# Kernel tuning notes

Hardware: AMD Instinct MI355X
Metric: run time of the kernel (lower is better)

The kernel has to match this reference:

```python
import jax, jax.numpy as jnp
import numpy as np

MARGIN = 1.0
EPS = 1e-12  # safe sqrt/normalize clamp; used entries have magnitude >> EPS


def _normalize(x):
    return x / jnp.maximum(jnp.linalg.norm(x, axis=-1, keepdims=True), EPS)


def _cdist(x, y):
    # Pairwise L2 distances, matches torch.cdist(p=2)
    sq = (jnp.sum(x * x, axis=-1)[:, None]
          + jnp.sum(y * y, axis=-1)[None, :]
          - 2.0 * (x @ y.T))
    return jnp.sqrt(jnp.maximum(sq, EPS))


def setup_inputs() -> dict:
    key = jax.random.key(0)
    k1, k2, k3 = jax.random.split(key, 3)
    B, P, D = 4096, 2, 256
    anchor = jax.random.normal(k1, (B, D), dtype=jnp.float32)
    positive = jax.random.normal(k2, (B, P, D), dtype=jnp.float32)
    labels = jax.random.randint(k3, (B,), 0, 200)
    return {"anchor": anchor, "positive": positive, "labels": labels}


def reference(anchor, positive, labels):
    a = _normalize(anchor)            # [B, D]
    p = _normalize(positive)          # [B, P, D]
    B = a.shape[0]
    all_labels = jnp.concatenate([labels, labels])           # [2B]
    neg_mask = all_labels[None, :] != labels[:, None]        # [B, 2B]
    idx = jnp.arange(B)
    losses = []
    for v in range(p.shape[1]):  # loop over small fixed num_positives
        feats = jnp.concatenate([a, p[:, v]], axis=0)        # [2B, D]
        dist = _cdist(feats, feats)                          # [2B, 2B]
        pos_dist = dist[idx, idx + B]                        # [B]
        # hard negative mining: min distance over different-label columns
        neg_dist = jnp.min(jnp.where(neg_mask, dist[:B], jnp.inf), axis=1)  # [B]
        losses.append(jnp.maximum(pos_dist - neg_dist + MARGIN, 0.0))
    return jnp.mean(jnp.stack(losses))
```

## Files before the change

kernel.cpp:

```cpp
#include <hip/hip_runtime.h>
#include <hip/hip_bf16.h>

#define NB    4096
#define ND    256
#define NP    2
#define TOT   (NB * 3)
#define RB    256
#define NCHUNK 48
#define COLS_PER_CHUNK (TOT / NCHUNK)
#define TILES (COLS_PER_CHUNK / 16)
#define PITCH 264
#define NEG_INIT (-4.0f)

typedef float f32x4 __attribute__((ext_vector_type(4)));

#define WS_F_OFF    0
#define WS_POS_OFF  (TOT * RB)
#define WS_PART_OFF (WS_POS_OFF + NB * NP * 4)

__global__ void norm_pos_kernel(const float* __restrict__ anchor,
                                const float* __restrict__ positive,
                                unsigned char* __restrict__ F,
                                float* __restrict__ posArr) {
    int wid = threadIdx.x >> 6, lane = threadIdx.x & 63;
    int row = blockIdx.x * 4 + wid;
    if (row < NB) {
        const float* src = anchor + (size_t)row * ND;
        float4 x = *(const float4*)(src + lane * 4);
        float ss = x.x * x.x + x.y * x.y + x.z * x.z + x.w * x.w;
        #pragma unroll
        for (int m = 1; m < 64; m <<= 1) ss += __shfl_xor(ss, m, 64);
        float inv = 1.0f / fmaxf(sqrtf(ss), 1e-12f);
        int pk = __builtin_amdgcn_cvt_pk_fp8_f32(x.x * inv, x.y * inv, 0, false);
        pk = __builtin_amdgcn_cvt_pk_fp8_f32(x.z * inv, x.w * inv, pk, true);
        *(int*)(F + (size_t)row * RB + lane * 4) = pk;
    } else {
        int q = row - NB;
        int v = q >> 12;
        int j = q & (NB - 1);
        const float* sp = positive + (size_t)(j * NP + v) * ND;
        const float* sa = anchor + (size_t)j * ND;
        float4 xp = *(const float4*)(sp + lane * 4);
        float4 xa = *(const float4*)(sa + lane * 4);
        float sspv = xp.x * xp.x + xp.y * xp.y + xp.z * xp.z + xp.w * xp.w;
        float ssa  = xa.x * xa.x + xa.y * xa.y + xa.z * xa.z + xa.w * xa.w;
        float dot  = xa.x * xp.x + xa.y * xp.y + xa.z * xp.z + xa.w * xp.w;
        #pragma unroll
        for (int m = 1; m < 64; m <<= 1) {
            sspv += __shfl_xor(sspv, m, 64);
            ssa  += __shfl_xor(ssa, m, 64);
            dot  += __shfl_xor(dot, m, 64);
        }
        float invp = 1.0f / fmaxf(sqrtf(sspv), 1e-12f);
        int pk = __builtin_amdgcn_cvt_pk_fp8_f32(xp.x * invp, xp.y * invp, 0, false);
        pk = __builtin_amdgcn_cvt_pk_fp8_f32(xp.z * invp, xp.w * invp, pk, true);
        *(int*)(F + (size_t)row * RB + lane * 4) = pk;
        if (lane == 0) {
            float inva = 1.0f / fmaxf(sqrtf(ssa), 1e-12f);
            float dn = dot * inva * invp;
            float sq = 2.0f - 2.0f * dn;
            posArr[j * NP + v] = sqrtf(fmaxf(sq, 1e-12f));
        }
    }
}

__global__ __launch_bounds__(256) void gram_max_kernel(
        const unsigned char* __restrict__ F,
        const int* __restrict__ labels,
        float* __restrict__ partials) {
    __shared__ unsigned char lds[2][16 * PITCH];
    __shared__ int slab[COLS_PER_CHUNK];
    int tid = threadIdx.x;
    int wid = tid >> 6, lane = tid & 63;
    int l15 = lane & 15, quad = lane >> 4;

    int id = blockIdx.x;
    int chunk = id >> 4;
    int rbi   = id & 15;

    int rowBase = rbi * 256 + wid * 64;
    int col0 = chunk * COLS_PER_CHUNK;
    int part = col0 >> 12;
    const unsigned char* Fb = F;

    slab[tid] = labels[(col0 & (NB - 1)) + tid];

    int scol = tid >> 4, sseg = tid & 15;

    long af[4][8];
    #pragma unroll
    for (int s = 0; s < 4; ++s) {
        const unsigned char* ar = Fb + (size_t)(rowBase + s * 16 + l15) * RB + quad * 8;
        #pragma unroll
        for (int kk = 0; kk < 8; ++kk)
            af[s][kk] = *(const long*)(ar + kk * 32);
    }
    unsigned rlp[4];
    #pragma unroll
    for (int s = 0; s < 4; ++s) {
        const int* lb = labels + rowBase + s * 16 + quad * 4;
        rlp[s] = (unsigned)lb[0] | ((unsigned)lb[1] << 8)
               | ((unsigned)lb[2] << 16) | ((unsigned)lb[3] << 24);
    }

    float vmax[4][4];
    #pragma unroll
    for (int s = 0; s < 4; ++s)
        #pragma unroll
        for (int r = 0; r < 4; ++r) vmax[s][r] = NEG_INIT;

    float4 r0;
    auto gload = [&](int ct) {
        const unsigned char* g = Fb + (size_t)(col0 + ct * 16 + scol) * RB + sseg * 16;
        r0 = *(const float4*)g;
    };
    auto swrite = [&](int buf) {
        *(float4*)&lds[buf][scol * PITCH + sseg * 16] = r0;
    };

    gload(0); swrite(0);
    gload(1);
    __syncthreads();

    for (int ct = 0; ct < TILES; ++ct) {
        int buf = ct & 1;
        long bfr[8];
        #pragma unroll
        for (int kk = 0; kk < 8; ++kk)
            bfr[kk] = *(const long*)&lds[buf][l15 * PITCH + quad * 8 + kk * 32];

        if (ct + 1 < TILES) swrite(buf ^ 1);
        if (ct + 2 < TILES) gload(ct + 2);

        int lc = slab[ct * 16 + l15];
        unsigned lcq = (unsigned)lc * 0x01010101u;

        f32x4 acc[4];
        #pragma unroll
        for (int s = 0; s < 4; ++s) acc[s] = (f32x4){0.f, 0.f, 0.f, 0.f};
        #pragma unroll
        for (int kk = 0; kk < 8; ++kk)
            #pragma unroll
            for (int s = 0; s < 4; ++s)
                acc[s] = __builtin_amdgcn_mfma_f32_16x16x32_fp8_fp8(af[s][kk], bfr[kk], acc[s], 0, 0, 0);

        #pragma unroll
        for (int s = 0; s < 4; ++s) {
            unsigned x = rlp[s] ^ lcq;
            #pragma unroll
            for (int r = 0; r < 4; ++r) {
                bool neq = ((x >> (8 * r)) & 0xffu) != 0u;
                vmax[s][r] = fmaxf(vmax[s][r], neq ? acc[s][r] : NEG_INIT);
            }
        }
        __syncthreads();
    }

    #pragma unroll
    for (int m = 1; m < 16; m <<= 1)
        #pragma unroll
        for (int s = 0; s < 4; ++s)
            #pragma unroll
            for (int r = 0; r < 4; ++r)
                vmax[s][r] = fmaxf(vmax[s][r], __shfl_xor(vmax[s][r], m, 64));

    if (l15 == 0) {
        #pragma unroll
        for (int s = 0; s < 4; ++s)
            #pragma unroll
            for (int r = 0; r < 4; ++r) {
                int row = rowBase + s * 16 + quad * 4 + r;
                partials[(size_t)part * NB * 16 + (size_t)row * 16 + (chunk & 15)] = vmax[s][r];
            }
    }
}

__global__ void finalize_kernel(const float* __restrict__ partials,
                                const float* __restrict__ posArr,
                                float* __restrict__ out) {
    int row = blockIdx.x * 256 + threadIdx.x;
    const float* pa = partials + (size_t)row * 16;
    const float* pb = pa + (size_t)NB * 16;
    const float* pc = pb + (size_t)NB * 16;
    float ma = NEG_INIT, m0 = NEG_INIT, m1 = NEG_INIT;
    #pragma unroll
    for (int j = 0; j < 16; ++j) {
        ma = fmaxf(ma, pa[j]);
        m0 = fmaxf(m0, pb[j]);
        m1 = fmaxf(m1, pc[j]);
    }
    float n0 = sqrtf(fmaxf(2.0f - 2.0f * fmaxf(ma, m0), 1e-12f));
    float n1 = sqrtf(fmaxf(2.0f - 2.0f * fmaxf(ma, m1), 1e-12f));
    float l = fmaxf(posArr[row * 2 + 0] - n0 + 1.0f, 0.0f)
            + fmaxf(posArr[row * 2 + 1] - n1 + 1.0f, 0.0f);
    int lane = threadIdx.x & 63, wid = threadIdx.x >> 6;
    #pragma unroll
    for (int m = 1; m < 64; m <<= 1) l += __shfl_xor(l, m, 64);
    __shared__ float wsum[4];
    if (lane == 0) wsum[wid] = l;
    __syncthreads();
    if (threadIdx.x == 0) {
        float s = wsum[0] + wsum[1] + wsum[2] + wsum[3];
        atomicAdd(out, s * (1.0f / (NB * NP)));
    }
}

extern "C" void kernel_launch(void* const* d_in, const int* in_sizes, int n_in,
                              void* d_out, int out_size, void* d_ws, size_t ws_size,
                              hipStream_t stream) {
    const float* anchor   = (const float*)d_in[0];
    const float* positive = (const float*)d_in[1];
    const int*   labels   = (const int*)d_in[2];
    float* out = (float*)d_out;

    unsigned char* F = (unsigned char*)((char*)d_ws + WS_F_OFF);
    float* posArr    = (float*)((char*)d_ws + WS_POS_OFF);
    float* partials  = (float*)((char*)d_ws + WS_PART_OFF);

    norm_pos_kernel<<<TOT / 4, 256, 0, stream>>>(anchor, positive, F, posArr);
    gram_max_kernel<<<(NB / 256) * NCHUNK, 256, 0, stream>>>(F, labels, partials);
    hipMemsetAsync(d_out, 0, sizeof(float), stream);
    finalize_kernel<<<NB / 256, 256, 0, stream>>>(partials, posArr, out);
}
```

Measured before the change: 100.5 us.

## Preload whole column chunk into swizzled LDS and drop per-tile syncs

The double-buffered per-tile global-to-LDS staging with a barrier every tile is replaced by a single up-front load of the block's whole 256-column chunk into LDS. The data is laid out in MFMA fragment order, so each lane reads its B operand as a contiguous 8-byte slot with no padding and no bank conflicts. This removes the per-tile __syncthreads and the serialized load/store pipeline. The cost is 64KB of LDS per block and an exposed initial load with no overlap, with launch bounds hinting at 2 blocks per CU.

```diff
diff --git a/kernel.cpp b/kernel.cpp
--- a/kernel.cpp
+++ b/kernel.cpp
@@ -7,12 +7,12 @@
 #define TOT   (NB * 3)
 #define RB    256
 #define NCHUNK 48
-#define COLS_PER_CHUNK (TOT / NCHUNK)
+#define COLS_PER_CHUNK 256
 #define TILES (COLS_PER_CHUNK / 16)
-#define PITCH 264
 #define NEG_INIT (-4.0f)
 
 typedef float f32x4 __attribute__((ext_vector_type(4)));
+typedef long  longx2 __attribute__((ext_vector_type(2)));
 
 #define WS_F_OFF    0
 #define WS_POS_OFF  (TOT * RB)
@@ -64,11 +64,11 @@
     }
 }
 
-__global__ __launch_bounds__(256) void gram_max_kernel(
+__global__ __launch_bounds__(256, 2) void gram_max_kernel(
         const unsigned char* __restrict__ F,
         const int* __restrict__ labels,
         float* __restrict__ partials) {
-    __shared__ unsigned char lds[2][16 * PITCH];
+    __shared__ unsigned char ldsB[TILES * 4096];
     __shared__ int slab[COLS_PER_CHUNK];
     int tid = threadIdx.x;
     int wid = tid >> 6, lane = tid & 63;
@@ -80,12 +80,8 @@
 
     int rowBase = rbi * 256 + wid * 64;
     int col0 = chunk * COLS_PER_CHUNK;
-    int part = col0 >> 12;
+    int part = chunk >> 4;
     const unsigned char* Fb = F;
-
-    slab[tid] = labels[(col0 & (NB - 1)) + tid];
-
-    int scol = tid >> 4, sseg = tid & 15;
 
     long af[4][8];
     #pragma unroll
@@ -103,34 +99,36 @@
                | ((unsigned)lb[2] << 16) | ((unsigned)lb[3] << 24);
     }
 
+    slab[tid] = labels[(col0 & (NB - 1)) + tid];
+    {
+        const unsigned char* g = Fb + (size_t)(col0 + tid) * RB;
+        int tilec = tid >> 4, c15 = tid & 15;
+        unsigned char* dbase = ldsB + tilec * 4096 + c15 * 8;
+        #pragma unroll
+        for (int kk = 0; kk < 8; ++kk) {
+            longx2 u = *(const longx2*)(g + kk * 32);
+            longx2 v = *(const longx2*)(g + kk * 32 + 16);
+            unsigned char* d = dbase + kk * 512;
+            *(long*)(d + 0 * 128) = u.x;
+            *(long*)(d + 1 * 128) = u.y;
+            *(long*)(d + 2 * 128) = v.x;
+            *(long*)(d + 3 * 128) = v.y;
+        }
+    }
+    __syncthreads();
+
     float vmax[4][4];
     #pragma unroll
     for (int s = 0; s < 4; ++s)
         #pragma unroll
         for (int r = 0; r < 4; ++r) vmax[s][r] = NEG_INIT;
 
-    float4 r0;
-    auto gload = [&](int ct) {
-        const unsigned char* g = Fb + (size_t)(col0 + ct * 16 + scol) * RB + sseg * 16;
-        r0 = *(const float4*)g;
-    };
-    auto swrite = [&](int buf) {
-        *(float4*)&lds[buf][scol * PITCH + sseg * 16] = r0;
-    };
-
-    gload(0); swrite(0);
-    gload(1);
-    __syncthreads();
-
+    #pragma unroll 2
     for (int ct = 0; ct < TILES; ++ct) {
-        int buf = ct & 1;
         long bfr[8];
         #pragma unroll
         for (int kk = 0; kk < 8; ++kk)
-            bfr[kk] = *(const long*)&lds[buf][l15 * PITCH + quad * 8 + kk * 32];
-
-        if (ct + 1 < TILES) swrite(buf ^ 1);
-        if (ct + 2 < TILES) gload(ct + 2);
+            bfr[kk] = *(const long*)&ldsB[ct * 4096 + kk * 512 + lane * 8];
 
         int lc = slab[ct * 16 + l15];
         unsigned lcq = (unsigned)lc * 0x01010101u;
@@ -153,7 +151,6 @@
                 vmax[s][r] = fmaxf(vmax[s][r], neq ? acc[s][r] : NEG_INIT);
             }
         }
-        __syncthreads();
     }
 
     #pragma unroll
```

Result: faster. 95.31 us (-5.2%).
